# Performance work log

Hardware: AMD Instinct MI355X
Metric: run time of the kernel (lower is better)

The kernel has to match this reference:

```python
import jax, jax.numpy as jnp
import numpy as np

N = 65536        # nodes
E = 262144       # edges
EDGE_DIM = 16    # invariant edge feature dim
HIDDEN = 32      # radial MLP hidden dim
M1 = 8; M2 = 8   # input/output multiplicities
D1 = 4; D2 = 4   # input/output irrep dims (degrees [0,1] -> 1+3)
K1 = 4; K2 = 4   # basis ranks (paths)


def setup_inputs() -> dict:
    key = jax.random.key(0)
    ks = jax.random.split(key, 8)
    basis1 = jax.random.normal(ks[0], (E, D1, K1), jnp.float32)
    basis2 = jax.random.normal(ks[1], (E, K2, D2), jnp.float32)
    edge_feats = jax.random.normal(ks[2], (E, EDGE_DIM), jnp.float32)
    f = jax.random.normal(ks[3], (N, M1, D1), jnp.float32)
    src_idx = jax.random.randint(ks[4], (E,), 0, N)
    w1 = jax.random.normal(ks[5], (EDGE_DIM, HIDDEN), jnp.float32) / np.sqrt(EDGE_DIM).astype(np.float32)
    bias1 = jnp.zeros((HIDDEN,), jnp.float32)
    w2 = jax.random.normal(ks[6], (HIDDEN, M2 * K2 * M1 * K1), jnp.float32) / np.sqrt(HIDDEN).astype(np.float32)
    bias2 = jnp.zeros((M2 * K2 * M1 * K1,), jnp.float32)
    return {"basis1": basis1, "basis2": basis2, "edge_feats": edge_feats,
            "f": f, "src_idx": src_idx, "w1": w1, "bias1": bias1,
            "w2": w2, "bias2": bias2}


def reference(basis1, basis2, edge_feats, f, src_idx, w1, bias1, w2, bias2):
    # Radial weight network (2-layer MLP, eval mode -> no dropout)
    h = jax.nn.relu(edge_feats @ w1 + bias1)                 # (E, HIDDEN)
    rw = (h @ w2 + bias2).reshape(E, M2 * K2, M1 * K1)       # (E, m2*k2, m1*k1)
    # Gather source node features per edge
    f_src = f[src_idx]                                       # (E, M1, D1)
    # Low-rank tensor-product contraction chain
    tmp = jnp.einsum('emd,edk->emk', f_src, basis1)          # (E, M1, K1)
    tmp = tmp.reshape(E, M1 * K1, 1)
    tmp = (rw @ tmp).reshape(E, M2, K2)                      # (E, M2, K2)
    return tmp @ basis2                                      # (E, M2, D2)
```

## Files before the change

kernel.cpp:

```cpp
#include <hip/hip_runtime.h>
#include <hip/hip_bf16.h>


#define TPB 512
#define BM  256

typedef __attribute__((ext_vector_type(8))) short bf16x8;
typedef __attribute__((ext_vector_type(4))) float f32x4;
typedef __attribute__((ext_vector_type(4))) unsigned int u32x4;

__device__ __forceinline__ ushort f2bf(float x) {
    __hip_bfloat16 b = __float2bfloat16(x);
    return __builtin_bit_cast(ushort, b);
}
__device__ __forceinline__ float bf2f(ushort u) {
    unsigned int v = ((unsigned int)u) << 16;
    return __builtin_bit_cast(float, v);
}
__device__ __forceinline__ unsigned int pack_trunc(float m0, float m1) {
    return __builtin_amdgcn_perm(__builtin_bit_cast(unsigned int, m1),
                                 __builtin_bit_cast(unsigned int, m0),
                                 0x07060302u);
}

__global__ __launch_bounds__(TPB, 6) void equiv_conv_mfma(
    const float* __restrict__ basis1,
    const float* __restrict__ basis2,
    const float* __restrict__ ef,
    const float* __restrict__ f,
    const int*   __restrict__ src_idx,
    const float* __restrict__ w1,
    const float* __restrict__ b1,
    const float* __restrict__ w2,
    const float* __restrict__ b2,
    float* __restrict__ out)
{
    __shared__ ushort hT[32 * BM];
    __shared__ ushort region[8192];

    ushort* tmpT = region;
    ushort* WL   = region;

    const int tid  = threadIdx.x;
    const int base = blockIdx.x * BM;

    const int jr2 = tid >> 6;
    const int tt2 = tid & 63;

    f32x4 stg[4];
    {
        const float* p = w2 + jr2 * 1024 + tt2 * 4;
        #pragma unroll
        for (int i = 0; i < 4; ++i)
            stg[i] = *reinterpret_cast<const f32x4*>(p + i * 256);
    }

    auto write_stage = [&]() {
        const int g   = (tt2 >> 1) & 3;
        const int i0v = (tt2 & 1) * 4;
        #pragma unroll
        for (int i = 0; i < 4; ++i) {
            const int a = i * 8 + (tt2 >> 3);
            unsigned int lo = (unsigned int)f2bf(stg[i][0]) | ((unsigned int)f2bf(stg[i][1]) << 16);
            unsigned int hi = (unsigned int)f2bf(stg[i][2]) | ((unsigned int)f2bf(stg[i][3]) << 16);
            *reinterpret_cast<uint2*>(&WL[jr2 * 1024 + g * 256 + a * 8 + i0v]) =
                make_uint2(lo, hi);
        }
    };

    if (tid < BM) {
        const int e = base + tid;
        {
            float efr[16];
            const f32x4* p4 = reinterpret_cast<const f32x4*>(ef + e * 16);
            #pragma unroll
            for (int i = 0; i < 4; ++i) {
                f32x4 v = p4[i];
                efr[i*4+0] = v[0]; efr[i*4+1] = v[1]; efr[i*4+2] = v[2]; efr[i*4+3] = v[3];
            }
            #pragma unroll
            for (int j = 0; j < 32; ++j) {
                float hv = b1[j];
                #pragma unroll
                for (int i = 0; i < 16; ++i)
                    hv = fmaf(efr[i], w1[i * 32 + j], hv);
                hT[j * BM + tid] = f2bf(fmaxf(hv, 0.f));
            }
        }
        {
            float fr[32];
            const int s = src_idx[e];
            const f32x4* p4 = reinterpret_cast<const f32x4*>(f + s * 32);
            #pragma unroll
            for (int i = 0; i < 8; ++i) {
                f32x4 v = p4[i];
                fr[i*4+0] = v[0]; fr[i*4+1] = v[1]; fr[i*4+2] = v[2]; fr[i*4+3] = v[3];
            }
            float bs1[16];
            const f32x4* q4 = reinterpret_cast<const f32x4*>(basis1 + e * 16);
            #pragma unroll
            for (int i = 0; i < 4; ++i) {
                f32x4 v = q4[i];
                bs1[i*4+0] = v[0]; bs1[i*4+1] = v[1]; bs1[i*4+2] = v[2]; bs1[i*4+3] = v[3];
            }
            float tmp[32];
            #pragma unroll
            for (int m = 0; m < 8; ++m) {
                #pragma unroll
                for (int k = 0; k < 4; ++k) {
                    float v = 0.f;
                    #pragma unroll
                    for (int d = 0; d < 4; ++d)
                        v = fmaf(fr[m*4+d], bs1[d*4+k], v);
                    tmp[m*4+k] = v;
                }
            }
            #pragma unroll
            for (int g = 0; g < 4; ++g) {
                uint4 pk;
                pk.x = (unsigned int)f2bf(tmp[g*8+0]) | ((unsigned int)f2bf(tmp[g*8+1]) << 16);
                pk.y = (unsigned int)f2bf(tmp[g*8+2]) | ((unsigned int)f2bf(tmp[g*8+3]) << 16);
                pk.z = (unsigned int)f2bf(tmp[g*8+4]) | ((unsigned int)f2bf(tmp[g*8+5]) << 16);
                pk.w = (unsigned int)f2bf(tmp[g*8+6]) | ((unsigned int)f2bf(tmp[g*8+7]) << 16);
                *reinterpret_cast<uint4*>(&tmpT[(g * BM + tid) * 8]) = pk;
            }
        }
    }

    __syncthreads();

    const int lane = tid & 63;
    const int wid  = tid >> 6;
    const int l15  = lane & 15;
    const int lg   = lane >> 4;

    float tmpf[2][8];
    #pragma unroll
    for (int q = 0; q < 2; ++q) {
        const int edge = wid * 32 + q * 16 + l15;
        bf16x8 tv = *reinterpret_cast<const bf16x8*>(&tmpT[(lg * BM + edge) * 8]);
        #pragma unroll
        for (int i = 0; i < 8; ++i) tmpf[q][i] = bf2f((ushort)tv[i]);
    }

    __syncthreads();
    write_stage();
    __syncthreads();

    f32x4 acc[2][2];
    #pragma unroll
    for (int q = 0; q < 2; ++q) {
        #pragma unroll
        for (int t = 0; t < 2; ++t) {
            acc[q][t][0] = 0.f; acc[q][t][1] = 0.f; acc[q][t][2] = 0.f; acc[q][t][3] = 0.f;
        }
    }

    #pragma unroll 1
    for (int c = 0; c < 4; ++c) {
        if (c < 3) {
            const float* p = w2 + ((c + 1) * 8 + jr2) * 1024 + tt2 * 4;
            #pragma unroll
            for (int i = 0; i < 4; ++i)
                stg[i] = *reinterpret_cast<const f32x4*>(p + i * 256);
        } else if (tid < 64) {
            const float* p = b2 + tt2 * 4;
            #pragma unroll
            for (int i = 0; i < 4; ++i)
                stg[i] = *reinterpret_cast<const f32x4*>(p + i * 256);
        }

        const ushort* Wb = WL;
        #pragma unroll
        for (int j8 = 0; j8 < 8; ++j8) {
            const int kk = c * 8 + j8;
            bf16x8 bf0 = *reinterpret_cast<const bf16x8*>(&Wb[j8 * 1024 + lg * 256 + l15 * 8]);
            bf16x8 bf1 = *reinterpret_cast<const bf16x8*>(&Wb[j8 * 1024 + lg * 256 + (16 + l15) * 8]);
            #pragma unroll
            for (int q = 0; q < 2; ++q) {
                const float hv = bf2f(hT[kk * BM + wid * 32 + q * 16 + l15]);
                u32x4 w;
                #pragma unroll
                for (int i = 0; i < 4; ++i)
                    w[i] = pack_trunc(hv * tmpf[q][2*i], hv * tmpf[q][2*i+1]);
                const bf16x8 af = __builtin_bit_cast(bf16x8, w);
                acc[q][0] = __builtin_amdgcn_mfma_f32_16x16x32_bf16(af, bf0, acc[q][0], 0, 0, 0);
                acc[q][1] = __builtin_amdgcn_mfma_f32_16x16x32_bf16(af, bf1, acc[q][1], 0, 0, 0);
            }
        }

        __syncthreads();
        if (c < 3) write_stage();
        else if (tid < 64) write_stage();
        __syncthreads();
    }

    {
        bf16x8 bb0 = *reinterpret_cast<const bf16x8*>(&WL[lg * 256 + l15 * 8]);
        bf16x8 bb1 = *reinterpret_cast<const bf16x8*>(&WL[lg * 256 + (16 + l15) * 8]);
        #pragma unroll
        for (int q = 0; q < 2; ++q) {
            u32x4 w;
            #pragma unroll
            for (int i = 0; i < 4; ++i)
                w[i] = pack_trunc(tmpf[q][2*i], tmpf[q][2*i+1]);
            const bf16x8 af = __builtin_bit_cast(bf16x8, w);
            acc[q][0] = __builtin_amdgcn_mfma_f32_16x16x32_bf16(af, bb0, acc[q][0], 0, 0, 0);
            acc[q][1] = __builtin_amdgcn_mfma_f32_16x16x32_bf16(af, bb1, acc[q][1], 0, 0, 0);
        }
    }

    const int k2  = lane & 3;
    const int m2l = (lane >> 2) & 3;
    #pragma unroll
    for (int q = 0; q < 2; ++q) {
        #pragma unroll
        for (int r = 0; r < 4; ++r) {
            const int eg = base + wid * 32 + q * 16 + lg * 4 + r;
            f32x4 bs2 = *reinterpret_cast<const f32x4*>(basis2 + eg * 16 + k2 * 4);
            #pragma unroll
            for (int t = 0; t < 2; ++t) {
                const float v = acc[q][t][r];
                float p0 = v * bs2[0], p1 = v * bs2[1], p2 = v * bs2[2], p3 = v * bs2[3];
                p0 += __shfl_xor(p0, 1); p0 += __shfl_xor(p0, 2);
                p1 += __shfl_xor(p1, 1); p1 += __shfl_xor(p1, 2);
                p2 += __shfl_xor(p2, 1); p2 += __shfl_xor(p2, 2);
                p3 += __shfl_xor(p3, 1); p3 += __shfl_xor(p3, 2);
                const float ov = (k2 == 0) ? p0 : (k2 == 1) ? p1 : (k2 == 2) ? p2 : p3;
                out[eg * 32 + (t * 4 + m2l) * 4 + k2] = ov;
            }
        }
    }
}

extern "C" void kernel_launch(void* const* d_in, const int* in_sizes, int n_in,
                              void* d_out, int out_size, void* d_ws, size_t ws_size,
                              hipStream_t stream) {
    const float* basis1 = (const float*)d_in[0];
    const float* basis2 = (const float*)d_in[1];
    const float* ef     = (const float*)d_in[2];
    const float* f      = (const float*)d_in[3];
    const int*   src    = (const int*)  d_in[4];
    const float* w1     = (const float*)d_in[5];
    const float* b1     = (const float*)d_in[6];
    const float* w2     = (const float*)d_in[7];
    const float* b2     = (const float*)d_in[8];
    float* out = (float*)d_out;

    const int E = in_sizes[4];
    const int nblocks = E / BM;

    equiv_conv_mfma<<<nblocks, TPB, 0, stream>>>(
        basis1, basis2, ef, f, src, w1, b1, w2, b2, out);
}
```

Before: 48.01 us.

## Prepack w2 to bf16 in workspace and stream MFMA B-operand from global

Adds a small pre-kernel that converts w2 and b2 to bf16 in the MFMA-ready layout in the workspace buffer, once per call. The main kernel then reads B fragments straight from global/L2 instead of staging each chunk through LDS with per-block conversion and barriers. This removes the chunk loop's __syncthreads and the redundant fp32-to-bf16 conversion in every block, at the cost of an extra launch and more global/L2 traffic per block. A fallback path keeps the old kernel when the workspace is too small.

```diff
diff --git a/kernel.cpp b/kernel.cpp
--- a/kernel.cpp
+++ b/kernel.cpp
@@ -23,7 +23,185 @@
                                  0x07060302u);
 }
 
-__global__ __launch_bounds__(TPB, 6) void equiv_conv_mfma(
+__global__ __launch_bounds__(256) void prep_w2(
+    const float* __restrict__ w2, const float* __restrict__ b2,
+    ushort* __restrict__ Bws)
+{
+    const int t = blockIdx.x * 256 + threadIdx.x;
+    if (t >= 33 * 128) return;
+    const int kk = t >> 7;
+    const int g  = (t >> 5) & 3;
+    const int a  = t & 31;
+    const float* src = (kk < 32) ? (w2 + kk * 1024 + a * 32 + g * 8)
+                                 : (b2 + a * 32 + g * 8);
+    f32x4 v0 = *reinterpret_cast<const f32x4*>(src);
+    f32x4 v1 = *reinterpret_cast<const f32x4*>(src + 4);
+    uint4 pk;
+    pk.x = (unsigned int)f2bf(v0[0]) | ((unsigned int)f2bf(v0[1]) << 16);
+    pk.y = (unsigned int)f2bf(v0[2]) | ((unsigned int)f2bf(v0[3]) << 16);
+    pk.z = (unsigned int)f2bf(v1[0]) | ((unsigned int)f2bf(v1[1]) << 16);
+    pk.w = (unsigned int)f2bf(v1[2]) | ((unsigned int)f2bf(v1[3]) << 16);
+    *reinterpret_cast<uint4*>(Bws + t * 8) = pk;
+}
+
+__global__ __launch_bounds__(TPB, 6) void equiv_conv_mfma_ws(
+    const float* __restrict__ basis1,
+    const float* __restrict__ basis2,
+    const float* __restrict__ ef,
+    const float* __restrict__ f,
+    const int*   __restrict__ src_idx,
+    const float* __restrict__ w1,
+    const float* __restrict__ b1,
+    const ushort* __restrict__ Bws,
+    float* __restrict__ out)
+{
+    __shared__ ushort hT[32 * BM];
+    __shared__ ushort tmpT[4 * BM * 8];
+
+    const int tid  = threadIdx.x;
+    const int base = blockIdx.x * BM;
+
+    if (tid < BM) {
+        const int e = base + tid;
+        {
+            float efr[16];
+            const f32x4* p4 = reinterpret_cast<const f32x4*>(ef + e * 16);
+            #pragma unroll
+            for (int i = 0; i < 4; ++i) {
+                f32x4 v = p4[i];
+                efr[i*4+0] = v[0]; efr[i*4+1] = v[1]; efr[i*4+2] = v[2]; efr[i*4+3] = v[3];
+            }
+            #pragma unroll
+            for (int j = 0; j < 32; ++j) {
+                float hv = b1[j];
+                #pragma unroll
+                for (int i = 0; i < 16; ++i)
+                    hv = fmaf(efr[i], w1[i * 32 + j], hv);
+                hT[j * BM + tid] = f2bf(fmaxf(hv, 0.f));
+            }
+        }
+        {
+            float fr[32];
+            const int s = src_idx[e];
+            const f32x4* p4 = reinterpret_cast<const f32x4*>(f + s * 32);
+            #pragma unroll
+            for (int i = 0; i < 8; ++i) {
+                f32x4 v = p4[i];
+                fr[i*4+0] = v[0]; fr[i*4+1] = v[1]; fr[i*4+2] = v[2]; fr[i*4+3] = v[3];
+            }
+            float bs1[16];
+            const f32x4* q4 = reinterpret_cast<const f32x4*>(basis1 + e * 16);
+            #pragma unroll
+            for (int i = 0; i < 4; ++i) {
+                f32x4 v = q4[i];
+                bs1[i*4+0] = v[0]; bs1[i*4+1] = v[1]; bs1[i*4+2] = v[2]; bs1[i*4+3] = v[3];
+            }
+            float tmp[32];
+            #pragma unroll
+            for (int m = 0; m < 8; ++m) {
+                #pragma unroll
+                for (int k = 0; k < 4; ++k) {
+                    float v = 0.f;
+                    #pragma unroll
+                    for (int d = 0; d < 4; ++d)
+                        v = fmaf(fr[m*4+d], bs1[d*4+k], v);
+                    tmp[m*4+k] = v;
+                }
+            }
+            #pragma unroll
+            for (int g = 0; g < 4; ++g) {
+                uint4 pk;
+                pk.x = (unsigned int)f2bf(tmp[g*8+0]) | ((unsigned int)f2bf(tmp[g*8+1]) << 16);
+                pk.y = (unsigned int)f2bf(tmp[g*8+2]) | ((unsigned int)f2bf(tmp[g*8+3]) << 16);
+                pk.z = (unsigned int)f2bf(tmp[g*8+4]) | ((unsigned int)f2bf(tmp[g*8+5]) << 16);
+                pk.w = (unsigned int)f2bf(tmp[g*8+6]) | ((unsigned int)f2bf(tmp[g*8+7]) << 16);
+                *reinterpret_cast<uint4*>(&tmpT[(g * BM + tid) * 8]) = pk;
+            }
+        }
+    }
+
+    __syncthreads();
+
+    const int lane = tid & 63;
+    const int wid  = tid >> 6;
+    const int l15  = lane & 15;
+    const int lg   = lane >> 4;
+
+    float tmpf[2][8];
+    #pragma unroll
+    for (int q = 0; q < 2; ++q) {
+        const int edge = wid * 32 + q * 16 + l15;
+        bf16x8 tv = *reinterpret_cast<const bf16x8*>(&tmpT[(lg * BM + edge) * 8]);
+        #pragma unroll
+        for (int i = 0; i < 8; ++i) tmpf[q][i] = bf2f((ushort)tv[i]);
+    }
+
+    f32x4 acc[2][2];
+    #pragma unroll
+    for (int q = 0; q < 2; ++q)
+        #pragma unroll
+        for (int t = 0; t < 2; ++t) {
+            acc[q][t][0] = 0.f; acc[q][t][1] = 0.f; acc[q][t][2] = 0.f; acc[q][t][3] = 0.f;
+        }
+
+    const bf16x8* Bp = reinterpret_cast<const bf16x8*>(Bws) + lg * 32 + l15;
+
+    #pragma unroll 4
+    for (int kk = 0; kk < 32; ++kk) {
+        bf16x8 bf0 = Bp[kk * 128];
+        bf16x8 bf1 = Bp[kk * 128 + 16];
+        #pragma unroll
+        for (int q = 0; q < 2; ++q) {
+            const float hv = bf2f(hT[kk * BM + wid * 32 + q * 16 + l15]);
+            u32x4 w;
+            #pragma unroll
+            for (int i = 0; i < 4; ++i)
+                w[i] = pack_trunc(hv * tmpf[q][2*i], hv * tmpf[q][2*i+1]);
+            const bf16x8 af = __builtin_bit_cast(bf16x8, w);
+            acc[q][0] = __builtin_amdgcn_mfma_f32_16x16x32_bf16(af, bf0, acc[q][0], 0, 0, 0);
+            acc[q][1] = __builtin_amdgcn_mfma_f32_16x16x32_bf16(af, bf1, acc[q][1], 0, 0, 0);
+        }
+    }
+
+    {
+        bf16x8 bb0 = Bp[32 * 128];
+        bf16x8 bb1 = Bp[32 * 128 + 16];
+        #pragma unroll
+        for (int q = 0; q < 2; ++q) {
+            u32x4 w;
+            #pragma unroll
+            for (int i = 0; i < 4; ++i)
+                w[i] = pack_trunc(tmpf[q][2*i], tmpf[q][2*i+1]);
+            const bf16x8 af = __builtin_bit_cast(bf16x8, w);
+            acc[q][0] = __builtin_amdgcn_mfma_f32_16x16x32_bf16(af, bb0, acc[q][0], 0, 0, 0);
+            acc[q][1] = __builtin_amdgcn_mfma_f32_16x16x32_bf16(af, bb1, acc[q][1], 0, 0, 0);
+        }
+    }
+
+    const int k2  = lane & 3;
+    const int m2l = (lane >> 2) & 3;
+    #pragma unroll
+    for (int q = 0; q < 2; ++q) {
+        #pragma unroll
+        for (int r = 0; r < 4; ++r) {
+            const int eg = base + wid * 32 + q * 16 + lg * 4 + r;
+            f32x4 bs2 = *reinterpret_cast<const f32x4*>(basis2 + eg * 16 + k2 * 4);
+            #pragma unroll
+            for (int t = 0; t < 2; ++t) {
+                const float v = acc[q][t][r];
+                float p0 = v * bs2[0], p1 = v * bs2[1], p2 = v * bs2[2], p3 = v * bs2[3];
+                p0 += __shfl_xor(p0, 1); p0 += __shfl_xor(p0, 2);
+                p1 += __shfl_xor(p1, 1); p1 += __shfl_xor(p1, 2);
+                p2 += __shfl_xor(p2, 1); p2 += __shfl_xor(p2, 2);
+                p3 += __shfl_xor(p3, 1); p3 += __shfl_xor(p3, 2);
+                const float ov = (k2 == 0) ? p0 : (k2 == 1) ? p1 : (k2 == 2) ? p2 : p3;
+                out[eg * 32 + (t * 4 + m2l) * 4 + k2] = ov;
+            }
+        }
+    }
+}
+
+__global__ __launch_bounds__(TPB, 6) void equiv_conv_mfma_fb(
     const float* __restrict__ basis1,
     const float* __restrict__ basis2,
     const float* __restrict__ ef,
@@ -37,16 +215,12 @@
 {
     __shared__ ushort hT[32 * BM];
     __shared__ ushort region[8192];
-
     ushort* tmpT = region;
     ushort* WL   = region;
-
     const int tid  = threadIdx.x;
     const int base = blockIdx.x * BM;
-
     const int jr2 = tid >> 6;
     const int tt2 = tid & 63;
-
     f32x4 stg[4];
     {
         const float* p = w2 + jr2 * 1024 + tt2 * 4;
@@ -54,7 +228,6 @@
         for (int i = 0; i < 4; ++i)
             stg[i] = *reinterpret_cast<const f32x4*>(p + i * 256);
     }
-
     auto write_stage = [&]() {
         const int g   = (tt2 >> 1) & 3;
         const int i0v = (tt2 & 1) * 4;
@@ -67,7 +240,6 @@
                 make_uint2(lo, hi);
         }
     };
-
     if (tid < BM) {
         const int e = base + tid;
         {
@@ -126,14 +298,11 @@
             }
         }
     }
-
     __syncthreads();
-
     const int lane = tid & 63;
     const int wid  = tid >> 6;
     const int l15  = lane & 15;
     const int lg   = lane >> 4;
-
     float tmpf[2][8];
     #pragma unroll
     for (int q = 0; q < 2; ++q) {
@@ -142,20 +311,16 @@
         #pragma unroll
         for (int i = 0; i < 8; ++i) tmpf[q][i] = bf2f((ushort)tv[i]);
     }
-
     __syncthreads();
     write_stage();
     __syncthreads();
-
     f32x4 acc[2][2];
     #pragma unroll
-    for (int q = 0; q < 2; ++q) {
+    for (int q = 0; q < 2; ++q)
         #pragma unroll
         for (int t = 0; t < 2; ++t) {
             acc[q][t][0] = 0.f; acc[q][t][1] = 0.f; acc[q][t][2] = 0.f; acc[q][t][3] = 0.f;
         }
-    }
-
     #pragma unroll 1
     for (int c = 0; c < 4; ++c) {
         if (c < 3) {
@@ -169,7 +334,6 @@
             for (int i = 0; i < 4; ++i)
                 stg[i] = *reinterpret_cast<const f32x4*>(p + i * 256);
         }
-
         const ushort* Wb = WL;
         #pragma unroll
         for (int j8 = 0; j8 < 8; ++j8) {
@@ -188,13 +352,11 @@
                 acc[q][1] = __builtin_amdgcn_mfma_f32_16x16x32_bf16(af, bf1, acc[q][1], 0, 0, 0);
             }
         }
-
         __syncthreads();
         if (c < 3) write_stage();
         else if (tid < 64) write_stage();
         __syncthreads();
     }
-
     {
         bf16x8 bb0 = *reinterpret_cast<const bf16x8*>(&WL[lg * 256 + l15 * 8]);
         bf16x8 bb1 = *reinterpret_cast<const bf16x8*>(&WL[lg * 256 + (16 + l15) * 8]);
@@ -209,7 +371,6 @@
             acc[q][1] = __builtin_amdgcn_mfma_f32_16x16x32_bf16(af, bb1, acc[q][1], 0, 0, 0);
         }
     }
-
     const int k2  = lane & 3;
     const int m2l = (lane >> 2) & 3;
     #pragma unroll
@@ -249,7 +410,15 @@
 
     const int E = in_sizes[4];
     const int nblocks = E / BM;
-
-    equiv_conv_mfma<<<nblocks, TPB, 0, stream>>>(
-        basis1, basis2, ef, f, src, w1, b1, w2, b2, out);
-}
+    const size_t need = (size_t)33 * 128 * 8 * sizeof(ushort);
+
+    if (ws_size >= need) {
+        ushort* Bws = (ushort*)d_ws;
+        prep_w2<<<17, 256, 0, stream>>>(w2, b2, Bws);
+        equiv_conv_mfma_ws<<<nblocks, TPB, 0, stream>>>(
+            basis1, basis2, ef, f, src, w1, b1, Bws, out);
+    } else {
+        equiv_conv_mfma_fb<<<nblocks, TPB, 0, stream>>>(
+            basis1, basis2, ef, f, src, w1, b1, w2, b2, out);
+    }
+}
```

After: 56.35 us. 17.4% more time.

## Split per-edge MLP layer-1 and basis1 contraction across all 512 threads

Applied to the files above, without the earlier changes.

Previously only the first 256 threads computed the first MLP layer and the f_src·basis1 contraction, one edge per thread, while the other half sat idle. Now each wave handles 32 edges, with the two half-waves splitting the 32 hidden units and the 8 input multiplicities between them. This halves the per-thread serial work and register pressure in the prologue. In exchange, edge_feats and basis1 are loaded twice per edge, once by each half.

```diff
diff --git a/kernel.cpp b/kernel.cpp
--- a/kernel.cpp
+++ b/kernel.cpp
@@ -68,69 +68,85 @@
         }
     };
 
-    if (tid < BM) {
-        const int e = base + tid;
-        {
-            float efr[16];
-            const f32x4* p4 = reinterpret_cast<const f32x4*>(ef + e * 16);
-            #pragma unroll
-            for (int i = 0; i < 4; ++i) {
-                f32x4 v = p4[i];
-                efr[i*4+0] = v[0]; efr[i*4+1] = v[1]; efr[i*4+2] = v[2]; efr[i*4+3] = v[3];
-            }
-            #pragma unroll
-            for (int j = 0; j < 32; ++j) {
-                float hv = b1[j];
-                #pragma unroll
-                for (int i = 0; i < 16; ++i)
-                    hv = fmaf(efr[i], w1[i * 32 + j], hv);
-                hT[j * BM + tid] = f2bf(fmaxf(hv, 0.f));
-            }
-        }
-        {
-            float fr[32];
-            const int s = src_idx[e];
-            const f32x4* p4 = reinterpret_cast<const f32x4*>(f + s * 32);
-            #pragma unroll
-            for (int i = 0; i < 8; ++i) {
-                f32x4 v = p4[i];
-                fr[i*4+0] = v[0]; fr[i*4+1] = v[1]; fr[i*4+2] = v[2]; fr[i*4+3] = v[3];
-            }
-            float bs1[16];
-            const f32x4* q4 = reinterpret_cast<const f32x4*>(basis1 + e * 16);
-            #pragma unroll
-            for (int i = 0; i < 4; ++i) {
-                f32x4 v = q4[i];
-                bs1[i*4+0] = v[0]; bs1[i*4+1] = v[1]; bs1[i*4+2] = v[2]; bs1[i*4+3] = v[3];
-            }
-            float tmp[32];
-            #pragma unroll
-            for (int m = 0; m < 8; ++m) {
-                #pragma unroll
-                for (int k = 0; k < 4; ++k) {
-                    float v = 0.f;
-                    #pragma unroll
-                    for (int d = 0; d < 4; ++d)
-                        v = fmaf(fr[m*4+d], bs1[d*4+k], v);
-                    tmp[m*4+k] = v;
-                }
-            }
-            #pragma unroll
-            for (int g = 0; g < 4; ++g) {
-                uint4 pk;
-                pk.x = (unsigned int)f2bf(tmp[g*8+0]) | ((unsigned int)f2bf(tmp[g*8+1]) << 16);
-                pk.y = (unsigned int)f2bf(tmp[g*8+2]) | ((unsigned int)f2bf(tmp[g*8+3]) << 16);
-                pk.z = (unsigned int)f2bf(tmp[g*8+4]) | ((unsigned int)f2bf(tmp[g*8+5]) << 16);
-                pk.w = (unsigned int)f2bf(tmp[g*8+6]) | ((unsigned int)f2bf(tmp[g*8+7]) << 16);
-                *reinterpret_cast<uint4*>(&tmpT[(g * BM + tid) * 8]) = pk;
-            }
-        }
-    }
-
-    __syncthreads();
-
     const int lane = tid & 63;
     const int wid  = tid >> 6;
+    const int el   = lane & 31;
+    const int half = lane >> 5;
+    const int e    = base + wid * 32 + el;
+
+    {
+        f32x4 ef4[4];
+        const f32x4* p4 = reinterpret_cast<const f32x4*>(ef + e * 16);
+        #pragma unroll
+        for (int i = 0; i < 4; ++i) ef4[i] = p4[i];
+
+        float hacc[16];
+        {
+            const f32x4* b14 = reinterpret_cast<const f32x4*>(b1 + half * 16);
+            #pragma unroll
+            for (int p = 0; p < 4; ++p) {
+                f32x4 b = b14[p];
+                hacc[p*4+0] = b[0]; hacc[p*4+1] = b[1];
+                hacc[p*4+2] = b[2]; hacc[p*4+3] = b[3];
+            }
+        }
+        #pragma unroll
+        for (int i = 0; i < 16; ++i) {
+            const float efi = ef4[i >> 2][i & 3];
+            const f32x4* w14 = reinterpret_cast<const f32x4*>(w1 + i * 32 + half * 16);
+            #pragma unroll
+            for (int p = 0; p < 4; ++p) {
+                f32x4 wv = w14[p];
+                hacc[p*4+0] = fmaf(efi, wv[0], hacc[p*4+0]);
+                hacc[p*4+1] = fmaf(efi, wv[1], hacc[p*4+1]);
+                hacc[p*4+2] = fmaf(efi, wv[2], hacc[p*4+2]);
+                hacc[p*4+3] = fmaf(efi, wv[3], hacc[p*4+3]);
+            }
+        }
+        #pragma unroll
+        for (int jj = 0; jj < 16; ++jj)
+            hT[(half * 16 + jj) * BM + wid * 32 + el] = f2bf(fmaxf(hacc[jj], 0.f));
+    }
+
+    {
+        const int s = src_idx[e];
+        f32x4 fr4[4];
+        const f32x4* p4 = reinterpret_cast<const f32x4*>(f + s * 32 + half * 16);
+        #pragma unroll
+        for (int i = 0; i < 4; ++i) fr4[i] = p4[i];
+        f32x4 b14[4];
+        const f32x4* q4 = reinterpret_cast<const f32x4*>(basis1 + e * 16);
+        #pragma unroll
+        for (int i = 0; i < 4; ++i) b14[i] = q4[i];
+
+        f32x4 acc4[4];
+        #pragma unroll
+        for (int ml = 0; ml < 4; ++ml) {
+            acc4[ml] = fr4[ml][0] * b14[0];
+            #pragma unroll
+            for (int d = 1; d < 4; ++d)
+                acc4[ml] += fr4[ml][d] * b14[d];
+        }
+        float tl[16];
+        #pragma unroll
+        for (int ml = 0; ml < 4; ++ml) {
+            tl[ml*4+0] = acc4[ml][0]; tl[ml*4+1] = acc4[ml][1];
+            tl[ml*4+2] = acc4[ml][2]; tl[ml*4+3] = acc4[ml][3];
+        }
+        #pragma unroll
+        for (int gl = 0; gl < 2; ++gl) {
+            uint4 pk;
+            pk.x = (unsigned int)f2bf(tl[gl*8+0]) | ((unsigned int)f2bf(tl[gl*8+1]) << 16);
+            pk.y = (unsigned int)f2bf(tl[gl*8+2]) | ((unsigned int)f2bf(tl[gl*8+3]) << 16);
+            pk.z = (unsigned int)f2bf(tl[gl*8+4]) | ((unsigned int)f2bf(tl[gl*8+5]) << 16);
+            pk.w = (unsigned int)f2bf(tl[gl*8+6]) | ((unsigned int)f2bf(tl[gl*8+7]) << 16);
+            *reinterpret_cast<uint4*>(
+                &tmpT[((half * 2 + gl) * BM + wid * 32 + el) * 8]) = pk;
+        }
+    }
+
+    __syncthreads();
+
     const int l15  = lane & 15;
     const int lg   = lane >> 4;
 
```

Measured after the change: 51.41 us. 7.1% more time.
